# Kernel tuning notes

Measured on AMD Instinct MI355X. Metric: run time of the kernel, lower is better.

## Reference

```python
import jax, jax.numpy as jnp
import numpy as np

T, B, C = 2048, 4, 512
H, K, P = 16, 31, 15  # num_heads, kernel_size, padding_l
R = C // H


def setup_inputs() -> dict:
    key = jax.random.key(0)
    ks = jax.random.split(key, 6)
    x = jax.random.normal(ks[0], (T, B, C), dtype=jnp.float32)
    s = 0.02
    W1 = jax.random.normal(ks[1], (C, C), dtype=jnp.float32) * s   # linear1 weight
    b1 = jnp.zeros((C,), dtype=jnp.float32)
    Wl = jax.random.normal(ks[2], (H * K, C), dtype=jnp.float32) * s  # weight_linear (no bias)
    W2 = jax.random.normal(ks[3], (C, C), dtype=jnp.float32) * s   # linear2 weight
    b2 = jnp.zeros((C,), dtype=jnp.float32)
    return {"x": x, "W1": W1, "b1": b1, "Wl": Wl, "W2": W2, "b2": b2}


def _dynamic_conv(h, Wl):
    # h: (T, B, C). Generate per-position per-head filters, softmax over K,
    # then banded weighted sum over a local window of K timesteps.
    w = jnp.einsum('tbc,kc->tbk', h, Wl).reshape(T, B, H, K)
    w = jax.nn.softmax(w, axis=-1)                      # weight_softmax=True
    # pad left P, right K-1-P ("same" window: position t sees h[t-P : t-P+K])
    hp = jnp.pad(h, ((P, K - 1 - P), (0, 0), (0, 0)))   # (T+K-1, B, C)
    idx = jnp.arange(T)[:, None] + jnp.arange(K)[None, :]  # (T, K)
    hw = hp[idx].reshape(T, K, B, H, R)                 # unfolded windows
    return jnp.einsum('tkbhr,tbhk->tbhr', hw, w).reshape(T, B, C)


def reference(x, W1, b1, Wl, W2, b2):
    h = jnp.einsum('tbc,dc->tbd', x, W1) + b1           # linear1 (glu=False -> no act)
    out = _dynamic_conv(h, Wl)                          # conv_bias=False
    out = jnp.einsum('tbc,dc->tbd', out, W2) + b2       # linear2
    return out
```

## Files before the change

kernel.cpp:

```cpp
#include <hip/hip_runtime.h>
#include <hip/hip_bf16.h>

#define TT 2048
#define BB 4
#define CC 512
#define HH 16
#define KK 31
#define PP 15
#define MM (TT*BB)
#define NPAD 512

typedef __bf16 bf16x8 __attribute__((ext_vector_type(8)));
typedef float f32x4 __attribute__((ext_vector_type(4)));
typedef unsigned short ushort8 __attribute__((ext_vector_type(8)));
typedef unsigned short ushort4v __attribute__((ext_vector_type(4)));

__device__ __forceinline__ float bf2f(unsigned short u) {
    return __uint_as_float(((unsigned int)u) << 16);
}
__device__ __forceinline__ unsigned short f2bf(float f) {
    unsigned int x = __float_as_uint(f);
    x += 0x7fffu + ((x >> 16) & 1u);
    return (unsigned short)(x >> 16);
}

__global__ __launch_bounds__(256) void cast_x(const float* __restrict__ src,
                                              unsigned short* __restrict__ dst) {
    const int i = (blockIdx.x * 256 + threadIdx.x) * 4;
    const float4 v = *(const float4*)&src[i];
    ushort4v o = { f2bf(v.x), f2bf(v.y), f2bf(v.z), f2bf(v.w) };
    *(ushort4v*)&dst[i] = o;
}

__global__ __launch_bounds__(256) void cast_weights(const float* __restrict__ W1,
                                                    const float* __restrict__ Wl,
                                                    const float* __restrict__ W2,
                                                    unsigned short* __restrict__ W1b,
                                                    unsigned short* __restrict__ Wlb,
                                                    unsigned short* __restrict__ W2b) {
    const int b = blockIdx.x;
    const int i = (b & 255) * 1024 + threadIdx.x * 4;
    const float* src;
    unsigned short* dst;
    int n_src = 262144;
    if (b < 256)      { src = W1; dst = W1b; }
    else if (b < 512) { src = Wl; dst = Wlb; n_src = HH * KK * CC; }
    else              { src = W2; dst = W2b; }
    ushort4v o = {0, 0, 0, 0};
    if (i < n_src) {
        const float4 v = *(const float4*)&src[i];
        o[0] = f2bf(v.x); o[1] = f2bf(v.y); o[2] = f2bf(v.z); o[3] = f2bf(v.w);
    }
    *(ushort4v*)&dst[i] = o;
}

#define GBM 128
#define GBN 64
#define GBK 64
#define KC  512
#define NT  8

#define STAGE(kt, buf)                                                                         \
    do {                                                                                       \
        const int k0_ = (kt) * GBK;                                                            \
        _Pragma("unroll")                                                                      \
        for (int j = 0; j < 4; ++j)                                                            \
            __builtin_amdgcn_global_load_lds(                                                  \
                (const __attribute__((address_space(1))) void*)(gA[j] + k0_),                  \
                (__attribute__((address_space(3))) void*)(&As[buf][0] + j * 2048 + wv * 512),  \
                16, 0, 0);                                                                     \
        _Pragma("unroll")                                                                      \
        for (int j = 0; j < 2; ++j)                                                            \
            __builtin_amdgcn_global_load_lds(                                                  \
                (const __attribute__((address_space(1))) void*)(gB[j] + k0_),                  \
                (__attribute__((address_space(3))) void*)(&Bs[buf][0] + j * 2048 + wv * 512),  \
                16, 0, 0);                                                                     \
    } while (0)

template<bool OUT_BF16>
__global__ __launch_bounds__(256, 2) void gemm_nt_mfma(const unsigned short* __restrict__ A,
                                                       const unsigned short* __restrict__ B,
                                                       const float* __restrict__ bias,
                                                       void* __restrict__ Cout,
                                                       int N, int nn) {
    __shared__ short As[3][GBM * GBK];
    __shared__ short Bs[3][GBN * GBK];

    const int tid = threadIdx.x;
    const int l   = tid & 63;
    const int wv  = tid >> 6;
    const int wr  = wv >> 1;
    const int wc  = wv & 1;

    const int s  = (blockIdx.x & 7) * (gridDim.x >> 3) + (blockIdx.x >> 3);
    const int bm = (s / nn) * GBM;
    const int bn = (s % nn) * GBN;

    const unsigned short* gA[4];
    const unsigned short* gB[2];
    #pragma unroll
    for (int j = 0; j < 4; ++j) {
        const int idx16 = j * 256 + tid;
        const int r  = idx16 >> 3;
        const int sl = (idx16 & 7) ^ (r & 7);
        gA[j] = A + (size_t)(bm + r) * KC + sl * 8;
    }
    #pragma unroll
    for (int j = 0; j < 2; ++j) {
        const int idx16 = j * 256 + tid;
        const int r  = idx16 >> 3;
        const int sl = (idx16 & 7) ^ (r & 7);
        gB[j] = B + (size_t)(bn + r) * KC + sl * 8;
    }

    f32x4 acc[4][2] = {};

    const int lr = l & 15;
    const int ls = l >> 4;
    int offA[4][2], offB[2][2];
    #pragma unroll
    for (int mi = 0; mi < 4; ++mi) {
        const int r = wr * 64 + mi * 16 + lr;
        #pragma unroll
        for (int ks = 0; ks < 2; ++ks)
            offA[mi][ks] = r * 64 + (((ks * 4 + ls) ^ (r & 7)) * 8);
    }
    #pragma unroll
    for (int ni = 0; ni < 2; ++ni) {
        const int r = wc * 32 + ni * 16 + lr;
        #pragma unroll
        for (int ks = 0; ks < 2; ++ks)
            offB[ni][ks] = r * 64 + (((ks * 4 + ls) ^ (r & 7)) * 8);
    }

    STAGE(0, 0);
    STAGE(1, 1);

    #pragma unroll
    for (int kt = 0; kt < NT; ++kt) {
        if (kt < NT - 1) asm volatile("s_waitcnt vmcnt(6)" ::: "memory");
        else             asm volatile("s_waitcnt vmcnt(0)" ::: "memory");
        __builtin_amdgcn_s_barrier();
        if (kt + 2 < NT) STAGE(kt + 2, (kt + 2) % 3);

        const int cb = kt % 3;
        bf16x8 af[4][2], bfv[2][2];
        #pragma unroll
        for (int mi = 0; mi < 4; ++mi)
            #pragma unroll
            for (int ks = 0; ks < 2; ++ks)
                af[mi][ks] = *(const bf16x8*)&As[cb][offA[mi][ks]];
        #pragma unroll
        for (int ni = 0; ni < 2; ++ni)
            #pragma unroll
            for (int ks = 0; ks < 2; ++ks)
                bfv[ni][ks] = *(const bf16x8*)&Bs[cb][offB[ni][ks]];

        #pragma unroll
        for (int mi = 0; mi < 4; ++mi)
            #pragma unroll
            for (int ni = 0; ni < 2; ++ni)
                #pragma unroll
                for (int ks = 0; ks < 2; ++ks)
                    acc[mi][ni] = __builtin_amdgcn_mfma_f32_16x16x32_bf16(af[mi][ks], bfv[ni][ks], acc[mi][ni], 0, 0, 0);
    }

    #pragma unroll
    for (int mi = 0; mi < 4; ++mi) {
        const int row0 = bm + wr * 64 + mi * 16 + ls * 4;
        #pragma unroll
        for (int ni = 0; ni < 2; ++ni) {
            const int col = bn + wc * 32 + ni * 16 + lr;
            const float bv = bias ? bias[col] : 0.0f;
            #pragma unroll
            for (int j = 0; j < 4; ++j) {
                const float v = acc[mi][ni][j] + bv;
                if (OUT_BF16)
                    ((unsigned short*)Cout)[(size_t)(row0 + j) * N + col] = f2bf(v);
                else
                    ((float*)Cout)[(size_t)(row0 + j) * N + col] = v;
            }
        }
    }
}

__global__ __launch_bounds__(64) void dynconv_fused(const unsigned short* __restrict__ hb,
                                                    const unsigned short* __restrict__ lgb,
                                                    unsigned short* __restrict__ cvb) {
    __shared__ float w_s[64][33];

    const int bid = blockIdx.x;
    const int u   = (bid & 7) * 256 + (bid >> 3);
    const int tg  = u >> 2;
    const int b   = u & 3;
    const int t0  = tg * 4;
    const int tid = threadIdx.x;

    {
        const int dt = tid >> 4, hd = tid & 15;
        const unsigned short* lp = lgb + (size_t)((t0 + dt) * BB + b) * NPAD + hd * KK;
        float e[KK];
        float mx = -1e30f;
        #pragma unroll
        for (int k = 0; k < KK; ++k) { e[k] = bf2f(lp[k]); mx = fmaxf(mx, e[k]); }
        float sm = 0.f;
        #pragma unroll
        for (int k = 0; k < KK; ++k) { e[k] = __expf(e[k] - mx); sm += e[k]; }
        const float inv = 1.f / sm;
        #pragma unroll
        for (int k = 0; k < KK; ++k) w_s[tid][k] = e[k] * inv;
    }
    __syncthreads();

    const int c0 = tid * 8;
    const int hd = tid >> 2;
    float acc[4][8] = {};
    #pragma unroll
    for (int j = 0; j < 34; ++j) {
        const int tt = t0 - PP + j;
        if ((unsigned)tt >= TT) continue;
        const ushort8 hv = *(const ushort8*)&hb[(size_t)((tt * BB + b) * CC) + c0];
        float hf[8];
        #pragma unroll
        for (int cc = 0; cc < 8; ++cc) hf[cc] = bf2f(hv[cc]);
        #pragma unroll
        for (int dt = 0; dt < 4; ++dt) {
            const int k = j - dt;
            if (k < 0 || k >= KK) continue;
            const float wk = w_s[dt * 16 + hd][k];
            #pragma unroll
            for (int cc = 0; cc < 8; ++cc) acc[dt][cc] = fmaf(hf[cc], wk, acc[dt][cc]);
        }
    }
    #pragma unroll
    for (int dt = 0; dt < 4; ++dt) {
        ushort8 o;
        #pragma unroll
        for (int cc = 0; cc < 8; ++cc) o[cc] = f2bf(acc[dt][cc]);
        *(ushort8*)&cvb[(size_t)(((t0 + dt) * BB + b) * CC) + c0] = o;
    }
}

extern "C" void kernel_launch(void* const* d_in, const int* in_sizes, int n_in,
                              void* d_out, int out_size, void* d_ws, size_t ws_size,
                              hipStream_t stream) {
    const float* x  = (const float*)d_in[0];
    const float* W1 = (const float*)d_in[1];
    const float* b1 = (const float*)d_in[2];
    const float* Wl = (const float*)d_in[3];
    const float* W2 = (const float*)d_in[4];
    const float* b2 = (const float*)d_in[5];
    float* out = (float*)d_out;

    unsigned short* xb  = (unsigned short*)d_ws;
    unsigned short* hb  = xb  + (size_t)MM * CC;
    unsigned short* cvb = hb  + (size_t)MM * CC;
    unsigned short* W1b = cvb + (size_t)MM * CC;
    unsigned short* Wlb = W1b + (size_t)CC * CC;
    unsigned short* W2b = Wlb + (size_t)NPAD * CC;
    unsigned short* lgb = W2b + (size_t)CC * CC;

    const int nxc = MM * CC;

    cast_x<<<nxc / 1024, 256, 0, stream>>>(x, xb);
    cast_weights<<<768, 256, 0, stream>>>(W1, Wl, W2, W1b, Wlb, W2b);

    const int nblk = (MM / GBM) * (CC / GBN);

    gemm_nt_mfma<true><<<nblk, 256, 0, stream>>>(xb, W1b, b1, hb, CC, CC / GBN);
    gemm_nt_mfma<true><<<nblk, 256, 0, stream>>>(hb, Wlb, nullptr, lgb, NPAD, NPAD / GBN);
    dynconv_fused<<<TT * BB / 4, 64, 0, stream>>>(hb, lgb, cvb);
    gemm_nt_mfma<false><<<nblk, 256, 0, stream>>>(cvb, W2b, b2, out, CC, CC / GBN);
}
```

Measured before the change: 54.03 us.

## Fold filter-logit projection into linear1 via precomputed combined weight

Precomputes Wl·W1 (a small GEMM on the weights) and a combined bias, so that h and the dynamic-conv logits come out of one GEMM over x with N=1024. This removes the serial dependency of the logits GEMM on h and avoids re-reading h from memory. In exchange it adds a W1 transpose kernel, a bias kernel and a tiny weight GEMM per call. It also changes rounding, because the logits are now computed from bf16(Wl·W1) rather than from bf16 h.

```diff
diff --git a/kernel.cpp b/kernel.cpp
--- a/kernel.cpp
+++ b/kernel.cpp
@@ -54,6 +54,51 @@
     *(ushort4v*)&dst[i] = o;
 }
 
+__global__ __launch_bounds__(256) void transpose_W1(const float* __restrict__ W1,
+                                                    unsigned short* __restrict__ W1t) {
+    __shared__ float t[64][65];
+    const int r16 = threadIdx.x >> 4;
+    const int c4  = (threadIdx.x & 15) * 4;
+    const int bd = blockIdx.y * 64, bc = blockIdx.x * 64;
+    #pragma unroll
+    for (int i = 0; i < 4; ++i) {
+        const int row = i * 16 + r16;
+        const float4 v = *(const float4*)&W1[(size_t)(bd + row) * 512 + bc + c4];
+        t[row][c4 + 0] = v.x; t[row][c4 + 1] = v.y;
+        t[row][c4 + 2] = v.z; t[row][c4 + 3] = v.w;
+    }
+    __syncthreads();
+    #pragma unroll
+    for (int i = 0; i < 4; ++i) {
+        const int orow = i * 16 + r16;
+        ushort4v o;
+        #pragma unroll
+        for (int j = 0; j < 4; ++j) o[j] = f2bf(t[c4 + j][orow]);
+        *(ushort4v*)&W1t[(size_t)(bc + orow) * 512 + bd + c4] = o;
+    }
+}
+
+__global__ __launch_bounds__(256) void make_bias(const float* __restrict__ b1,
+                                                 const float* __restrict__ Wl,
+                                                 float* __restrict__ bias_comb) {
+    const int bid = blockIdx.x, tid = threadIdx.x;
+    if (tid < 64) bias_comb[bid * 64 + tid] = b1[bid * 64 + tid];
+    const int r = bid * 64 + (tid >> 2);
+    const int q = tid & 3;
+    float sm = 0.f;
+    if (r < HH * KK) {
+        #pragma unroll
+        for (int j = 0; j < 32; ++j) {
+            const float4 wv = *(const float4*)&Wl[(size_t)r * 512 + q * 128 + j * 4];
+            const float4 bv = *(const float4*)&b1[q * 128 + j * 4];
+            sm += wv.x * bv.x + wv.y * bv.y + wv.z * bv.z + wv.w * bv.w;
+        }
+    }
+    sm += __shfl_xor(sm, 1, 4);
+    sm += __shfl_xor(sm, 2, 4);
+    if (q == 0) bias_comb[512 + r] = sm;
+}
+
 #define GBM 128
 #define GBN 64
 #define GBK 64
@@ -77,11 +122,12 @@
                 16, 0, 0);                                                                     \
     } while (0)
 
-template<bool OUT_BF16>
+template<int MODE>
 __global__ __launch_bounds__(256, 2) void gemm_nt_mfma(const unsigned short* __restrict__ A,
                                                        const unsigned short* __restrict__ B,
                                                        const float* __restrict__ bias,
                                                        void* __restrict__ Cout,
+                                                       void* __restrict__ Cout2,
                                                        int N, int nn) {
     __shared__ short As[3][GBM * GBK];
     __shared__ short Bs[3][GBN * GBK];
@@ -175,10 +221,16 @@
             #pragma unroll
             for (int j = 0; j < 4; ++j) {
                 const float v = acc[mi][ni][j] + bv;
-                if (OUT_BF16)
+                if (MODE == 0) {
+                    ((float*)Cout)[(size_t)(row0 + j) * N + col] = v;
+                } else if (MODE == 1) {
                     ((unsigned short*)Cout)[(size_t)(row0 + j) * N + col] = f2bf(v);
-                else
-                    ((float*)Cout)[(size_t)(row0 + j) * N + col] = v;
+                } else {
+                    unsigned short* dst = (col < 512) ? (unsigned short*)Cout
+                                                      : (unsigned short*)Cout2;
+                    const int c2 = (col < 512) ? col : col - 512;
+                    dst[(size_t)(row0 + j) * 512 + c2] = f2bf(v);
+                }
             }
         }
     }
@@ -252,23 +304,26 @@
     const float* b2 = (const float*)d_in[5];
     float* out = (float*)d_out;
 
-    unsigned short* xb  = (unsigned short*)d_ws;
-    unsigned short* hb  = xb  + (size_t)MM * CC;
-    unsigned short* cvb = hb  + (size_t)MM * CC;
-    unsigned short* W1b = cvb + (size_t)MM * CC;
-    unsigned short* Wlb = W1b + (size_t)CC * CC;
-    unsigned short* W2b = Wlb + (size_t)NPAD * CC;
-    unsigned short* lgb = W2b + (size_t)CC * CC;
+    unsigned short* xb    = (unsigned short*)d_ws;
+    unsigned short* hb    = xb  + (size_t)MM * CC;
+    unsigned short* cvb   = hb  + (size_t)MM * CC;
+    unsigned short* lgb   = cvb + (size_t)MM * CC;
+    unsigned short* Wcomb = lgb + (size_t)MM * CC;
+    unsigned short* Wlb   = Wcomb + (size_t)1024 * CC;
+    unsigned short* W1t   = Wlb + (size_t)NPAD * CC;
+    unsigned short* W2b   = W1t + (size_t)CC * CC;
+    float*          biasc = (float*)(W2b + (size_t)CC * CC);
 
     const int nxc = MM * CC;
 
     cast_x<<<nxc / 1024, 256, 0, stream>>>(x, xb);
-    cast_weights<<<768, 256, 0, stream>>>(W1, Wl, W2, W1b, Wlb, W2b);
-
-    const int nblk = (MM / GBM) * (CC / GBN);
-
-    gemm_nt_mfma<true><<<nblk, 256, 0, stream>>>(xb, W1b, b1, hb, CC, CC / GBN);
-    gemm_nt_mfma<true><<<nblk, 256, 0, stream>>>(hb, Wlb, nullptr, lgb, NPAD, NPAD / GBN);
+    cast_weights<<<768, 256, 0, stream>>>(W1, Wl, W2, Wcomb, Wlb, W2b);
+    transpose_W1<<<dim3(8, 8), 256, 0, stream>>>(W1, W1t);
+    make_bias<<<8, 256, 0, stream>>>(b1, Wl, biasc);
+
+    gemm_nt_mfma<1><<<32, 256, 0, stream>>>(Wlb, W1t, nullptr,
+                                            Wcomb + (size_t)512 * CC, nullptr, CC, 8);
+    gemm_nt_mfma<2><<<1024, 256, 0, stream>>>(xb, Wcomb, biasc, hb, lgb, 1024, 16);
     dynconv_fused<<<TT * BB / 4, 64, 0, stream>>>(hb, lgb, cvb);
-    gemm_nt_mfma<false><<<nblk, 256, 0, stream>>>(cvb, W2b, b2, out, CC, CC / GBN);
-}
+    gemm_nt_mfma<0><<<512, 256, 0, stream>>>(cvb, W2b, b2, out, nullptr, CC, 8);
+}
```

After: 72.83 us. 1.35x slower.
